# Kernel optimization log

Hardware: AMD Instinct MI355X
Metric: run time of the kernel (lower is better)

## Reference

```python
import jax, jax.numpy as jnp
import numpy as np

# dims
B, C, H, W = 2, 256, 128, 256
P, G = 9, 8            # num_pts, num_groups
GC = C // G            # group_channels


def setup_inputs() -> dict:
    key = jax.random.key(0)
    ks = jax.random.split(key, 8)
    s = 0.02
    return {
        "feats1": jax.random.normal(ks[0], (B, C, H, W), jnp.float32),
        "feats2": jax.random.normal(ks[1], (B, C, H, W), jnp.float32),
        "anchor_points": jax.random.uniform(ks[2], (B, H * W, 2), jnp.float32),
        "norm1_g": jnp.ones((C,), jnp.float32), "norm1_b": jnp.zeros((C,), jnp.float32),
        "norm2_g": jnp.ones((C,), jnp.float32), "norm2_b": jnp.zeros((C,), jnp.float32),
        "Wv": jax.random.normal(ks[3], (C, C), jnp.float32) * s, "bv": jnp.zeros((C,), jnp.float32),
        "Ww": jax.random.normal(ks[4], (C, G * P), jnp.float32) * s, "bw": jnp.zeros((G * P,), jnp.float32),
        "Wk": jax.random.normal(ks[5], (C, P), jnp.float32) * s, "bk": jnp.zeros((P,), jnp.float32),
        "Wo": jax.random.normal(ks[6], (C, C), jnp.float32) * s, "bo": jnp.zeros((C,), jnp.float32),
    }


def _ln(x, g, b):
    # LayerNorm over the last (channel) axis, eps as torch default
    m = jnp.mean(x, axis=-1, keepdims=True)
    v = jnp.mean(jnp.square(x - m), axis=-1, keepdims=True)
    return (x - m) * jax.lax.rsqrt(v + 1e-5) * g + b


def _bilinear_sample(value, pts):
    # value: (b, H, W, C); pts: (b, N, 2) normalized [0,1] (x, y)
    # grid_sample semantics: align_corners=False, zero padding
    b, h, w, c = value.shape
    x = pts[..., 0] * w - 0.5
    y = pts[..., 1] * h - 0.5
    x0 = jnp.floor(x)
    y0 = jnp.floor(y)
    wx = (x - x0)[..., None]
    wy = (y - y0)[..., None]
    x0i = x0.astype(jnp.int32)
    y0i = y0.astype(jnp.int32)
    vflat = value.reshape(b, h * w, c)

    def gather(yi, xi):
        valid = (yi >= 0) & (yi < h) & (xi >= 0) & (xi < w)
        idx = jnp.clip(yi, 0, h - 1) * w + jnp.clip(xi, 0, w - 1)
        g = jnp.take_along_axis(vflat, idx[..., None], axis=1)
        return g * valid[..., None].astype(value.dtype)

    v00 = gather(y0i, x0i)
    v01 = gather(y0i, x0i + 1)
    v10 = gather(y0i + 1, x0i)
    v11 = gather(y0i + 1, x0i + 1)
    return (v00 * (1 - wx) * (1 - wy) + v01 * wx * (1 - wy)
            + v10 * (1 - wx) * wy + v11 * wx * wy)


def reference(feats1, feats2, anchor_points, norm1_g, norm1_b, norm2_g, norm2_b,
              Wv, bv, Ww, bw, Wk, bk, Wo, bo):
    b, c, h, w = feats1.shape
    hw = h * w
    # to_3d(dim=2): (b, c, h, w) -> (b, hw, c); LayerNorm over c
    x1 = _ln(feats1.reshape(b, c, hw).transpose(0, 2, 1), norm1_g, norm1_b)
    x2 = _ln(feats2.reshape(b, c, hw).transpose(0, 2, 1), norm2_g, norm2_b)

    # value_proj (1x1 conv == per-pixel linear)
    value = (x2 @ Wv + bv).reshape(b, h, w, c)

    # weight_proj -> (b, hw, P, G); channel layout p*G + g; softmax over the P points per group
    logits = (x1 @ Ww + bw).reshape(b, hw, P, G)
    wts = jax.nn.softmax(logits, axis=2)

    # 1D key-point generator: per-pixel learned offsets along x around the anchor
    off = x1 @ Wk + bk                                   # (b, hw, P) normalized offsets
    kx = anchor_points[..., 0:1] + off                   # (b, hw, P)
    ky = jnp.broadcast_to(anchor_points[..., 1:2], kx.shape)
    kp = jnp.stack([kx, ky], axis=-1)                    # (b, hw, P, 2)

    # deformable aggregation: bilinear gather + group-weighted sum over points
    samp = _bilinear_sample(value, kp.reshape(b, hw * P, 2)).reshape(b, hw, P, G, GC)
    agg = jnp.einsum('bnpgc,bnpg->bngc', samp, wts).reshape(b, hw, c)

    out = (agg @ Wo + bo).reshape(b, h, w, c).transpose(0, 3, 1, 2)  # (b, c, h, w)
    return out, kp.reshape(b, h, w, P, 2)
```

## Files before the change

### kernel.cpp

```cpp
#include <hip/hip_runtime.h>
#include <hip/hip_bf16.h>


constexpr int B = 2, C = 256, H = 128, W = 256;
constexpr int HW = H * W;
constexpr int P = 9, G = 8;
constexpr int PIX = 32;
constexpr int NPIX = B * HW;
constexpr int NBKT = 2 * 129;

typedef __attribute__((ext_vector_type(8))) __bf16 bf16x8;
typedef __attribute__((ext_vector_type(4))) float f32x4;
typedef __attribute__((ext_vector_type(2))) float f32x2;
typedef __attribute__((ext_vector_type(2))) __fp16 fp16x2;

static __device__ __forceinline__ unsigned short f2bf(float x) {
    __hip_bfloat16 h = __float2bfloat16(x);
    return *reinterpret_cast<unsigned short*>(&h);
}
static __device__ __forceinline__ unsigned int pack2(float a, float b) {
    return (unsigned int)f2bf(a) | ((unsigned int)f2bf(b) << 16);
}
static __device__ __forceinline__ unsigned int pkh(float a, float b) {
    fp16x2 h = __builtin_amdgcn_cvt_pkrtz(a, b);
    return *reinterpret_cast<unsigned int*>(&h);
}
static __device__ __forceinline__ float bf2f(unsigned short u) {
    return __uint_as_float((unsigned int)u << 16);
}
static __device__ __forceinline__ bf16x8 ldb8g(const unsigned short* p) {
    return *reinterpret_cast<const bf16x8*>(p);
}

#define FMA_LO(acc, pk, c) \
    asm("v_fma_mix_f32 %0, %1, %2, %0 op_sel:[0,0,0] op_sel_hi:[1,0,0]" \
        : "+v"(acc) : "v"(pk), "v"(c))
#define FMA_HI(acc, pk, c) \
    asm("v_fma_mix_f32 %0, %1, %2, %0 op_sel:[1,0,0] op_sel_hi:[1,0,0]" \
        : "+v"(acc) : "v"(pk), "v"(c))

__global__ __launch_bounds__(256) void k_prep(
    const float* __restrict__ Ww, const float* __restrict__ Wv,
    const float* __restrict__ Wo,
    unsigned short* __restrict__ WwT, unsigned short* __restrict__ WvT,
    unsigned short* __restrict__ WoT)
{
    int tid = blockIdx.x * 256 + threadIdx.x;
    if (tid < 20480) {
        int n = tid >> 8, k = tid & 255;
        WwT[tid] = f2bf((n < 72) ? Ww[k * 72 + n] : 0.f);
    } else if (tid < 20480 + 65536) {
        int i = tid - 20480;
        int n = i >> 8, k = i & 255;
        WvT[i] = f2bf(Wv[k * 256 + n]);
    } else {
        int i = tid - 86016;
        int n = i >> 8, k = i & 255;
        WoT[i] = f2bf(Wo[k * 256 + n]);
    }
}

static __device__ __forceinline__ int bucket_of(const float* anchor, int pix) {
    float ay = anchor[(size_t)pix * 2 + 1];
    int y0 = (int)floorf(ay * (float)H - 0.5f);
    y0 = min(max(y0, -1), H - 1);
    return (pix >> 15) * 129 + y0 + 1;
}

__global__ __launch_bounds__(1024) void k_hist(
    const float* __restrict__ anchor, int* __restrict__ hist64)
{
    __shared__ int h[NBKT];
    const int t = threadIdx.x, blk = blockIdx.x;
    for (int i = t; i < NBKT; i += 1024) h[i] = 0;
    __syncthreads();
    atomicAdd(&h[bucket_of(anchor, blk * 1024 + t)], 1);
    __syncthreads();
    for (int i = t; i < NBKT; i += 1024) hist64[blk * NBKT + i] = h[i];
}

__global__ __launch_bounds__(256) void k_scan(
    const int* __restrict__ hist64, int* __restrict__ off)
{
    __shared__ int tot[NBKT], base[NBKT];
    const int t = threadIdx.x;
    for (int bkt = t; bkt < NBKT; bkt += 256) {
        int run = 0;
        for (int blk = 0; blk < 64; ++blk) run += hist64[blk * NBKT + bkt];
        tot[bkt] = run;
    }
    __syncthreads();
    if (t == 0) {
        int run = 0;
        for (int i = 0; i < NBKT; ++i) { base[i] = run; run += tot[i]; }
    }
    __syncthreads();
    for (int bkt = t; bkt < NBKT; bkt += 256) {
        int run = base[bkt];
        for (int blk = 0; blk < 64; ++blk) {
            int v = hist64[blk * NBKT + bkt];
            off[blk * NBKT + bkt] = run;
            run += v;
        }
    }
}

__global__ __launch_bounds__(1024) void k_scatter(
    const float* __restrict__ anchor, const int* __restrict__ off,
    int* __restrict__ perm)
{
    __shared__ int cur[NBKT];
    const int t = threadIdx.x, blk = blockIdx.x;
    for (int i = t; i < NBKT; i += 1024) cur[i] = off[blk * NBKT + i];
    __syncthreads();
    int pix = blk * 1024 + t;
    int pos = atomicAdd(&cur[bucket_of(anchor, pix)], 1);
    perm[pos] = pix;
}

__global__ __launch_bounds__(256) void kA(
    const float* __restrict__ feats1, const float* __restrict__ anchor,
    const float* __restrict__ g1, const float* __restrict__ b1,
    const float* __restrict__ Wk, const float* __restrict__ bk,
    const unsigned short* __restrict__ WwT, const float* __restrict__ bw,
    unsigned short* __restrict__ wtsb, float* __restrict__ kp_out)
{
    __shared__ unsigned short Hi[PIX][264];
    __shared__ __align__(16) char smB[20480];
    __shared__ float meanA[PIX], rstdA[PIX], axL[PIX], ayL[PIX];

    float* WkL  = (float*)smB;
    float* red2 = (float*)(smB + 9216);
    float* red  = (float*)(smB + 18432);
    float* Lg   = (float*)smB;

    const int t = threadIdx.x;
    const int p = t & 31;
    const int part = t >> 5;
    const int gpix0 = blockIdx.x * PIX;
    const int b = gpix0 >> 15;
    const int n0 = gpix0 & (HW - 1);
    const float* Fb = feats1 + (size_t)b * C * HW;

    for (int i = t; i < 2304; i += 256) WkL[i] = Wk[i];
    if (t < PIX) {
        axL[t] = anchor[((size_t)gpix0 + t) * 2 + 0];
        ayL[t] = anchor[((size_t)gpix0 + t) * 2 + 1];
    }

    float x[32];
    #pragma unroll
    for (int i = 0; i < 32; ++i)
        x[i] = Fb[(size_t)(part * 32 + i) * HW + n0 + p];

    float s = 0.f, ss = 0.f;
    #pragma unroll
    for (int i = 0; i < 32; ++i) { s += x[i]; ss += x[i] * x[i]; }
    red[part * 32 + p] = s;
    red[256 + part * 32 + p] = ss;
    __syncthreads();
    if (part == 0) {
        float s2 = 0.f, ss2 = 0.f;
        #pragma unroll
        for (int k = 0; k < 8; ++k) { s2 += red[k * 32 + p]; ss2 += red[256 + k * 32 + p]; }
        float mean = s2 * (1.f / C);
        float var  = ss2 * (1.f / C) - mean * mean;
        meanA[p] = mean; rstdA[p] = rsqrtf(var + 1e-5f);
    }
    __syncthreads();

    {
        float mean = meanA[p], rstd = rstdA[p];
        #pragma unroll
        for (int i = 0; i < 32; ++i) {
            int c = part * 32 + i;
            x[i] = (x[i] - mean) * rstd * g1[c] + b1[c];
        }
    }

    {
        float po[9];
        #pragma unroll
        for (int pt = 0; pt < 9; ++pt) po[pt] = 0.f;
        #pragma unroll 4
        for (int i = 0; i < 32; ++i) {
            int c = part * 32 + i;
            float xv = x[i];
            #pragma unroll
            for (int pt = 0; pt < 9; ++pt) po[pt] += xv * WkL[c * 9 + pt];
        }
        #pragma unroll
        for (int pt = 0; pt < 9; ++pt) red2[(part * 32 + p) * 9 + pt] = po[pt];
    }

    {
        unsigned int* row = (unsigned int*)&Hi[p][part * 32];
        #pragma unroll
        for (int i = 0; i < 16; ++i) row[i] = pack2(x[2 * i], x[2 * i + 1]);
    }
    __syncthreads();

    for (int tau = t; tau < 288; tau += 256) {
        int px = tau & 31, pt = tau >> 5;
        float offv = bk[pt];
        #pragma unroll
        for (int k = 0; k < 8; ++k) offv += red2[(k * 32 + px) * 9 + pt];
        size_t o = (((size_t)gpix0 + px) * P + pt) * 2;
        kp_out[o] = axL[px] + offv;
        kp_out[o + 1] = ayL[px];
    }

    const int wave = t >> 6, lane = t & 63;
    const int l15 = lane & 15, quad = lane >> 4;
    const int mt = wave & 1;
    const int ntb = (wave >> 1) * 3;
    const int ntc = (wave >> 1) ? 2 : 3;

    f32x4 acc[3];
    #pragma unroll
    for (int j = 0; j < 3; ++j) acc[j] = (f32x4){0.f, 0.f, 0.f, 0.f};

    const unsigned short* arow = &Hi[mt * 16 + l15][quad * 8];
    for (int kk = 0; kk < 8; ++kk) {
        bf16x8 a = *reinterpret_cast<const bf16x8*>(arow + kk * 32);
        for (int j = 0; j < 3; ++j) {
            if (j < ntc) {
                bf16x8 bfr = ldb8g(WwT + (size_t)((ntb + j) * 16 + l15) * 256 + quad * 8 + kk * 32);
                acc[j] = __builtin_amdgcn_mfma_f32_16x16x32_bf16(a, bfr, acc[j], 0, 0, 0);
            }
        }
    }
    __syncthreads();

    #pragma unroll
    for (int j = 0; j < 3; ++j) {
        if (j < ntc) {
            int n = (ntb + j) * 16 + l15;
            if (n < 72) {
                float bwn = bw[n];
                #pragma unroll
                for (int r = 0; r < 4; ++r)
                    Lg[(mt * 16 + quad * 4 + r) * 81 + n] = acc[j][r] + bwn;
            }
        }
    }
    __syncthreads();

    {
        int px = t >> 3, g = t & 7;
        float m = -1e30f;
        #pragma unroll
        for (int pt = 0; pt < P; ++pt) m = fmaxf(m, Lg[px * 81 + pt * 8 + g]);
        float e[P], sum = 0.f;
        #pragma unroll
        for (int pt = 0; pt < P; ++pt) { e[pt] = __expf(Lg[px * 81 + pt * 8 + g] - m); sum += e[pt]; }
        float inv = 1.f / sum;
        unsigned short* wb = wtsb + ((size_t)gpix0 + px) * 72 + g * 9;
        #pragma unroll
        for (int pt = 0; pt < P; ++pt) wb[pt] = f2bf(e[pt] * inv);
    }
}

__global__ __launch_bounds__(256) void kB(
    const float* __restrict__ feats2,
    const float* __restrict__ g2, const float* __restrict__ b2,
    const unsigned short* __restrict__ WvT, const float* __restrict__ bv,
    unsigned short* __restrict__ val)
{
    __shared__ unsigned short Hi[PIX][264];
    __shared__ float red[2][8][PIX];
    __shared__ float meanA[PIX], rstdA[PIX];

    const int t = threadIdx.x;
    const int p = t & 31;
    const int part = t >> 5;
    const int gpix0 = blockIdx.x * PIX;
    const int b = gpix0 >> 15;
    const int n0 = gpix0 & (HW - 1);
    const float* Fb = feats2 + (size_t)b * C * HW;

    float x[32];
    #pragma unroll
    for (int i = 0; i < 32; ++i)
        x[i] = Fb[(size_t)(part * 32 + i) * HW + n0 + p];

    float s = 0.f, ss = 0.f;
    #pragma unroll
    for (int i = 0; i < 32; ++i) { s += x[i]; ss += x[i] * x[i]; }
    red[0][part][p] = s; red[1][part][p] = ss;
    __syncthreads();
    if (part == 0) {
        float s2 = 0.f, ss2 = 0.f;
        #pragma unroll
        for (int k = 0; k < 8; ++k) { s2 += red[0][k][p]; ss2 += red[1][k][p]; }
        float mean = s2 * (1.f / C);
        float var  = ss2 * (1.f / C) - mean * mean;
        meanA[p] = mean; rstdA[p] = rsqrtf(var + 1e-5f);
    }
    __syncthreads();
    {
        float mean = meanA[p], rstd = rstdA[p];
        unsigned int* row = (unsigned int*)&Hi[p][part * 32];
        #pragma unroll
        for (int i = 0; i < 16; ++i) {
            float v0 = (x[2 * i] - mean) * rstd * g2[part * 32 + 2 * i] + b2[part * 32 + 2 * i];
            float v1 = (x[2 * i + 1] - mean) * rstd * g2[part * 32 + 2 * i + 1] + b2[part * 32 + 2 * i + 1];
            row[i] = pack2(v0, v1);
        }
    }
    __syncthreads();

    const int wave = t >> 6, lane = t & 63;
    const int l15 = lane & 15, quad = lane >> 4;
    const int m0 = wave * 64;

    f32x4 acc[4][2];
    #pragma unroll
    for (int ms = 0; ms < 4; ++ms)
        #pragma unroll
        for (int nt = 0; nt < 2; ++nt)
            acc[ms][nt] = (f32x4){0.f, 0.f, 0.f, 0.f};

    for (int kk = 0; kk < 8; ++kk) {
        bf16x8 a[4], bfr[2];
        #pragma unroll
        for (int ms = 0; ms < 4; ++ms)
            a[ms] = ldb8g(WvT + (size_t)(m0 + ms * 16 + l15) * 256 + quad * 8 + kk * 32);
        #pragma unroll
        for (int nt = 0; nt < 2; ++nt)
            bfr[nt] = *reinterpret_cast<const bf16x8*>(&Hi[nt * 16 + l15][quad * 8 + kk * 32]);
        #pragma unroll
        for (int ms = 0; ms < 4; ++ms)
            #pragma unroll
            for (int nt = 0; nt < 2; ++nt)
                acc[ms][nt] = __builtin_amdgcn_mfma_f32_16x16x32_bf16(a[ms], bfr[nt], acc[ms][nt], 0, 0, 0);
    }

    #pragma unroll
    for (int ms = 0; ms < 4; ++ms) {
        int ch0 = m0 + ms * 16 + quad * 4;
        float b0 = bv[ch0], b1v = bv[ch0 + 1], b2v = bv[ch0 + 2], b3 = bv[ch0 + 3];
        #pragma unroll
        for (int nt = 0; nt < 2; ++nt) {
            int pix = gpix0 + nt * 16 + l15;
            uint2 o;
            o.x = pkh(acc[ms][nt][0] + b0, acc[ms][nt][1] + b1v);
            o.y = pkh(acc[ms][nt][2] + b2v, acc[ms][nt][3] + b3);
            *reinterpret_cast<uint2*>(val + (size_t)pix * 256 + ch0) = o;
        }
    }
}

__global__ __launch_bounds__(256, 4) void k_gather(
    const unsigned short* __restrict__ wtsb,
    const float* __restrict__ kp,
    const unsigned short* __restrict__ val,
    const int* __restrict__ perm,
    unsigned short* __restrict__ aggb)
{
    __shared__ int   CF[PIX][66];
    __shared__ float WL[PIX * 8 * 11];
    __shared__ float EY[PIX][2];
    __shared__ int pixL[PIX];

    const int t = threadIdx.x;
    const int phys = blockIdx.x;
    const int lb = (phys & 7) * 256 + (phys >> 3);
    const int gpix0 = lb * PIX;

    if (t < PIX) {
        int pix = perm[gpix0 + t];
        pixL[t] = pix;
        float ay = kp[(size_t)pix * 18 + 1];
        float yf = ay * (float)H - 0.5f;
        float y0f = floorf(yf);
        float wy = yf - y0f;
        int y0 = (int)y0f;
        EY[t][0] = (((unsigned)y0 < (unsigned)H) ? 1.f : 0.f) * (1.f - wy);
        EY[t][1] = (((unsigned)(y0 + 1) < (unsigned)H) ? 1.f : 0.f) * wy;
        int yb0 = min(max(y0, 0), H - 1) * W;
        int yb1 = min(max(y0 + 1, 0), H - 1) * W;
        int base = (pix >> 15) * HW;
        CF[t][54] = (base + yb0) << 9;
        CF[t][55] = (base + yb1) << 9;
    }
    __syncthreads();

    for (int tau = t; tau < 288; tau += 256) {
        int px = tau & 31, pt = tau >> 5;
        int pix = pixL[px];
        float kx = kp[(size_t)pix * 18 + 2 * pt];
        float e0 = EY[px][0], e1 = EY[px][1];
        float xf = kx * (float)W - 0.5f;
        float x0f = floorf(xf);
        float wx = xf - x0f;
        int x0 = (int)x0f;
        float g0 = (1.f - wx) * (((unsigned)x0 < (unsigned)W) ? 1.f : 0.f);
        float g1v = wx * (((unsigned)(x0 + 1) < (unsigned)W) ? 1.f : 0.f);
        CF[px][pt * 6 + 0] = __float_as_int(g0 * e0);
        CF[px][pt * 6 + 1] = __float_as_int(g1v * e0);
        CF[px][pt * 6 + 2] = __float_as_int(g0 * e1);
        CF[px][pt * 6 + 3] = __float_as_int(g1v * e1);
        CF[px][pt * 6 + 4] = min(max(x0, 0), W - 1) << 9;
        CF[px][pt * 6 + 5] = min(max(x0 + 1, 0), W - 1) << 9;
    }
    {
        int px = t >> 3, j = t & 7;
        int pix = pixL[px];
        const unsigned short* wrow = wtsb + (size_t)pix * 72 + j * 9;
        float* wl = &WL[(px * 8 + j) * 11];
        #pragma unroll
        for (int k = 0; k < 9; ++k) wl[k] = bf2f(wrow[k]);
    }
    __syncthreads();

    const int wave = t >> 6, lane = t & 63;
    const int gl = lane >> 3;
    const char* vb = (const char*)val;
    const unsigned lane8 = (unsigned)lane * 8u;

    for (int px = wave; px < PIX; px += 4) {
        int cw = CF[px][lane];
        unsigned rb0 = (unsigned)__builtin_amdgcn_readlane(cw, 54);
        unsigned rb1 = (unsigned)__builtin_amdgcn_readlane(cw, 55);
        const char* pr0 = vb + rb0;
        const char* pr1 = vb + rb1;
        const float* wl = &WL[(px * 8 + gl) * 11];

        uint2 q[9][4];
        #pragma unroll
        for (int pt = 0; pt < P; ++pt) {
            unsigned xb0 = (unsigned)__builtin_amdgcn_readlane(cw, pt * 6 + 4);
            unsigned xb1 = (unsigned)__builtin_amdgcn_readlane(cw, pt * 6 + 5);
            q[pt][0] = *(const uint2*)(pr0 + xb0 + lane8);
            q[pt][1] = *(const uint2*)(pr0 + xb1 + lane8);
            q[pt][2] = *(const uint2*)(pr1 + xb0 + lane8);
            q[pt][3] = *(const uint2*)(pr1 + xb1 + lane8);
        }

        float a0 = 0.f, a1 = 0.f, a2 = 0.f, a3 = 0.f;
        #pragma unroll
        for (int pt = 0; pt < P; ++pt) {
            float u00 = __int_as_float(__builtin_amdgcn_readlane(cw, pt * 6 + 0));
            float u01 = __int_as_float(__builtin_amdgcn_readlane(cw, pt * 6 + 1));
            float u10 = __int_as_float(__builtin_amdgcn_readlane(cw, pt * 6 + 2));
            float u11 = __int_as_float(__builtin_amdgcn_readlane(cw, pt * 6 + 3));
            float w = wl[pt];
            float c00 = w * u00, c01 = w * u01, c10 = w * u10, c11 = w * u11;

            FMA_LO(a0, q[pt][0].x, c00); FMA_HI(a1, q[pt][0].x, c00);
            FMA_LO(a2, q[pt][0].y, c00); FMA_HI(a3, q[pt][0].y, c00);
            FMA_LO(a0, q[pt][1].x, c01); FMA_HI(a1, q[pt][1].x, c01);
            FMA_LO(a2, q[pt][1].y, c01); FMA_HI(a3, q[pt][1].y, c01);
            FMA_LO(a0, q[pt][2].x, c10); FMA_HI(a1, q[pt][2].x, c10);
            FMA_LO(a2, q[pt][2].y, c10); FMA_HI(a3, q[pt][2].y, c10);
            FMA_LO(a0, q[pt][3].x, c11); FMA_HI(a1, q[pt][3].x, c11);
            FMA_LO(a2, q[pt][3].y, c11); FMA_HI(a3, q[pt][3].y, c11);
        }

        int pix = pixL[px];
        uint2 o;
        o.x = pack2(a0, a1);
        o.y = pack2(a2, a3);
        *reinterpret_cast<uint2*>(aggb + ((size_t)pix << 8) + 4 * lane) = o;
    }
}

__global__ __launch_bounds__(256) void k_gemmo(
    const unsigned short* __restrict__ aggb,
    const unsigned short* __restrict__ WoT,
    const float* __restrict__ bo,
    float* __restrict__ out)
{
    const int t = threadIdx.x;
    const int wave = t >> 6, lane = t & 63;
    const int n_base = blockIdx.x * 64;
    const int b = n_base >> 15;
    const int hw0 = n_base & (HW - 1);
    const int m0 = wave * 64;
    const int l15 = lane & 15, quad = lane >> 4;

    f32x4 acc[4][4];
    #pragma unroll
    for (int ms = 0; ms < 4; ++ms)
        #pragma unroll
        for (int ns = 0; ns < 4; ++ns)
            acc[ms][ns] = (f32x4){0.f, 0.f, 0.f, 0.f};

    size_t aoff[4], boff[4];
    #pragma unroll
    for (int ms = 0; ms < 4; ++ms)
        aoff[ms] = (size_t)(m0 + ms * 16 + l15) * 256 + quad * 8;
    #pragma unroll
    for (int ns = 0; ns < 4; ++ns)
        boff[ns] = (size_t)(n_base + ns * 16 + l15) * 256 + quad * 8;

    for (int kk = 0; kk < 8; ++kk) {
        bf16x8 a[4], bfr[4];
        #pragma unroll
        for (int ms = 0; ms < 4; ++ms) a[ms] = ldb8g(WoT + aoff[ms] + kk * 32);
        #pragma unroll
        for (int ns = 0; ns < 4; ++ns) bfr[ns] = ldb8g(aggb + boff[ns] + kk * 32);
        #pragma unroll
        for (int ms = 0; ms < 4; ++ms)
            #pragma unroll
            for (int ns = 0; ns < 4; ++ns)
                acc[ms][ns] = __builtin_amdgcn_mfma_f32_16x16x32_bf16(a[ms], bfr[ns], acc[ms][ns], 0, 0, 0);
    }

    float bor[4][4];
    #pragma unroll
    for (int ms = 0; ms < 4; ++ms)
        #pragma unroll
        for (int r = 0; r < 4; ++r)
            bor[ms][r] = bo[m0 + ms * 16 + quad * 4 + r];

    #pragma unroll
    for (int ms = 0; ms < 4; ++ms) {
        #pragma unroll
        for (int ns = 0; ns < 4; ++ns) {
            #pragma unroll
            for (int r = 0; r < 4; ++r) {
                int ch = m0 + ms * 16 + quad * 4 + r;
                out[((size_t)b * 256 + ch) * HW + hw0 + ns * 16 + l15] = acc[ms][ns][r] + bor[ms][r];
            }
        }
    }
}

extern "C" void kernel_launch(void* const* d_in, const int* in_sizes, int n_in,
                              void* d_out, int out_size, void* d_ws, size_t ws_size,
                              hipStream_t stream)
{
    const float* feats1 = (const float*)d_in[0];
    const float* feats2 = (const float*)d_in[1];
    const float* anchor = (const float*)d_in[2];
    const float* n1g    = (const float*)d_in[3];
    const float* n1b    = (const float*)d_in[4];
    const float* n2g    = (const float*)d_in[5];
    const float* n2b    = (const float*)d_in[6];
    const float* Wv     = (const float*)d_in[7];
    const float* bv     = (const float*)d_in[8];
    const float* Ww     = (const float*)d_in[9];
    const float* bw     = (const float*)d_in[10];
    const float* Wk     = (const float*)d_in[11];
    const float* bk     = (const float*)d_in[12];
    const float* Wo     = (const float*)d_in[13];
    const float* bo     = (const float*)d_in[14];

    float* out = (float*)d_out;
    float* kp  = out + (size_t)B * C * HW;

    char* ws = (char*)d_ws;
    unsigned short* val  = (unsigned short*)(ws);
    unsigned short* aggb = (unsigned short*)(ws + 33554432);
    unsigned short* wtsb = (unsigned short*)(ws + 67108864);
    unsigned short* WwT  = (unsigned short*)(ws + 76546048);
    unsigned short* WvT  = (unsigned short*)(ws + 76587008);
    unsigned short* WoT  = (unsigned short*)(ws + 76718080);
    int* perm   = (int*)(ws + 76849152);
    int* hist64 = (int*)(ws + 77111296);
    int* off    = (int*)(ws + 77375488);

    k_prep   <<<592,  256,  0, stream>>>(Ww, Wv, Wo, WwT, WvT, WoT);
    k_hist   <<<64,   1024, 0, stream>>>(anchor, hist64);
    k_scan   <<<1,    256,  0, stream>>>(hist64, off);
    k_scatter<<<64,   1024, 0, stream>>>(anchor, off, perm);
    kA       <<<2048, 256,  0, stream>>>(feats1, anchor, n1g, n1b, Wk, bk, WwT, bw, wtsb, kp);
    kB       <<<2048, 256,  0, stream>>>(feats2, n2g, n2b, WvT, bv, val);
    k_gather <<<2048, 256,  0, stream>>>(wtsb, kp, val, perm, aggb);
    k_gemmo  <<<1024, 256,  0, stream>>>(aggb, WoT, bo, out);
}
```

Baseline: 404.5 us.

## Software-pipeline gather loads across pixels in deformable aggregation kernel

New measurement: 404.2 us. No clear change (-0.1%).

```diff
diff --git a/kernel.cpp b/kernel.cpp
--- a/kernel.cpp
+++ b/kernel.cpp
@@ -348,6 +348,47 @@
             o.y = pkh(acc[ms][nt][2] + b2v, acc[ms][nt][3] + b3);
             *reinterpret_cast<uint2*>(val + (size_t)pix * 256 + ch0) = o;
         }
+    }
+}
+
+template <int PTBASE, int NPT>
+static __device__ __forceinline__ void issue_loads(
+    uint2* q, int cw, const char* pr0, const char* pr1, unsigned lane8)
+{
+    #pragma unroll
+    for (int j = 0; j < NPT; ++j) {
+        unsigned xb0 = (unsigned)__builtin_amdgcn_readlane(cw, (PTBASE + j) * 6 + 4);
+        unsigned xb1 = (unsigned)__builtin_amdgcn_readlane(cw, (PTBASE + j) * 6 + 5);
+        q[4 * j + 0] = *(const uint2*)(pr0 + xb0 + lane8);
+        q[4 * j + 1] = *(const uint2*)(pr0 + xb1 + lane8);
+        q[4 * j + 2] = *(const uint2*)(pr1 + xb0 + lane8);
+        q[4 * j + 3] = *(const uint2*)(pr1 + xb1 + lane8);
+    }
+}
+
+template <int PTBASE, int NPT>
+static __device__ __forceinline__ void fma_block(
+    const uint2* q, int cw, const float* wl,
+    float& a0, float& a1, float& a2, float& a3)
+{
+    #pragma unroll
+    for (int j = 0; j < NPT; ++j) {
+        const int pt = PTBASE + j;
+        float u00 = __int_as_float(__builtin_amdgcn_readlane(cw, pt * 6 + 0));
+        float u01 = __int_as_float(__builtin_amdgcn_readlane(cw, pt * 6 + 1));
+        float u10 = __int_as_float(__builtin_amdgcn_readlane(cw, pt * 6 + 2));
+        float u11 = __int_as_float(__builtin_amdgcn_readlane(cw, pt * 6 + 3));
+        float w = wl[pt];
+        float c00 = w * u00, c01 = w * u01, c10 = w * u10, c11 = w * u11;
+
+        FMA_LO(a0, q[4 * j + 0].x, c00); FMA_HI(a1, q[4 * j + 0].x, c00);
+        FMA_LO(a2, q[4 * j + 0].y, c00); FMA_HI(a3, q[4 * j + 0].y, c00);
+        FMA_LO(a0, q[4 * j + 1].x, c01); FMA_HI(a1, q[4 * j + 1].x, c01);
+        FMA_LO(a2, q[4 * j + 1].y, c01); FMA_HI(a3, q[4 * j + 1].y, c01);
+        FMA_LO(a0, q[4 * j + 2].x, c10); FMA_HI(a1, q[4 * j + 2].x, c10);
+        FMA_LO(a2, q[4 * j + 2].y, c10); FMA_HI(a3, q[4 * j + 2].y, c10);
+        FMA_LO(a0, q[4 * j + 3].x, c11); FMA_HI(a1, q[4 * j + 3].x, c11);
+        FMA_LO(a2, q[4 * j + 3].y, c11); FMA_HI(a3, q[4 * j + 3].y, c11);
     }
 }
 
@@ -419,50 +460,51 @@
     const char* vb = (const char*)val;
     const unsigned lane8 = (unsigned)lane * 8u;
 
-    for (int px = wave; px < PIX; px += 4) {
-        int cw = CF[px][lane];
-        unsigned rb0 = (unsigned)__builtin_amdgcn_readlane(cw, 54);
-        unsigned rb1 = (unsigned)__builtin_amdgcn_readlane(cw, 55);
+    uint2 qa[16], qb[20];
+
+    int px = wave;
+    int cwA = CF[px][lane];
+    {
+        unsigned rb0 = (unsigned)__builtin_amdgcn_readlane(cwA, 54);
+        unsigned rb1 = (unsigned)__builtin_amdgcn_readlane(cwA, 55);
         const char* pr0 = vb + rb0;
         const char* pr1 = vb + rb1;
+        issue_loads<0, 4>(qa, cwA, pr0, pr1, lane8);
+    }
+    unsigned rbA0 = (unsigned)__builtin_amdgcn_readlane(cwA, 54);
+    unsigned rbA1 = (unsigned)__builtin_amdgcn_readlane(cwA, 55);
+
+    for (int i = 0; i < 8; ++i) {
         const float* wl = &WL[(px * 8 + gl) * 11];
-
-        uint2 q[9][4];
-        #pragma unroll
-        for (int pt = 0; pt < P; ++pt) {
-            unsigned xb0 = (unsigned)__builtin_amdgcn_readlane(cw, pt * 6 + 4);
-            unsigned xb1 = (unsigned)__builtin_amdgcn_readlane(cw, pt * 6 + 5);
-            q[pt][0] = *(const uint2*)(pr0 + xb0 + lane8);
-            q[pt][1] = *(const uint2*)(pr0 + xb1 + lane8);
-            q[pt][2] = *(const uint2*)(pr1 + xb0 + lane8);
-            q[pt][3] = *(const uint2*)(pr1 + xb1 + lane8);
-        }
+        const char* pr0A = vb + rbA0;
+        const char* pr1A = vb + rbA1;
+
+        issue_loads<4, 5>(qb, cwA, pr0A, pr1A, lane8);
+        __builtin_amdgcn_sched_barrier(0);
 
         float a0 = 0.f, a1 = 0.f, a2 = 0.f, a3 = 0.f;
-        #pragma unroll
-        for (int pt = 0; pt < P; ++pt) {
-            float u00 = __int_as_float(__builtin_amdgcn_readlane(cw, pt * 6 + 0));
-            float u01 = __int_as_float(__builtin_amdgcn_readlane(cw, pt * 6 + 1));
-            float u10 = __int_as_float(__builtin_amdgcn_readlane(cw, pt * 6 + 2));
-            float u11 = __int_as_float(__builtin_amdgcn_readlane(cw, pt * 6 + 3));
-            float w = wl[pt];
-            float c00 = w * u00, c01 = w * u01, c10 = w * u10, c11 = w * u11;
-
-            FMA_LO(a0, q[pt][0].x, c00); FMA_HI(a1, q[pt][0].x, c00);
-            FMA_LO(a2, q[pt][0].y, c00); FMA_HI(a3, q[pt][0].y, c00);
-            FMA_LO(a0, q[pt][1].x, c01); FMA_HI(a1, q[pt][1].x, c01);
-            FMA_LO(a2, q[pt][1].y, c01); FMA_HI(a3, q[pt][1].y, c01);
-            FMA_LO(a0, q[pt][2].x, c10); FMA_HI(a1, q[pt][2].x, c10);
-            FMA_LO(a2, q[pt][2].y, c10); FMA_HI(a3, q[pt][2].y, c10);
-            FMA_LO(a0, q[pt][3].x, c11); FMA_HI(a1, q[pt][3].x, c11);
-            FMA_LO(a2, q[pt][3].y, c11); FMA_HI(a3, q[pt][3].y, c11);
-        }
+        fma_block<0, 4>(qa, cwA, wl, a0, a1, a2, a3);
+
+        int pxn = (i < 7) ? px + 4 : px;
+        int cwN = CF[pxn][lane];
+        unsigned rbN0 = (unsigned)__builtin_amdgcn_readlane(cwN, 54);
+        unsigned rbN1 = (unsigned)__builtin_amdgcn_readlane(cwN, 55);
+        {
+            const char* pr0N = vb + rbN0;
+            const char* pr1N = vb + rbN1;
+            issue_loads<0, 4>(qa, cwN, pr0N, pr1N, lane8);
+        }
+        __builtin_amdgcn_sched_barrier(0);
+
+        fma_block<4, 5>(qb, cwA, wl, a0, a1, a2, a3);
 
         int pix = pixL[px];
         uint2 o;
         o.x = pack2(a0, a1);
         o.y = pack2(a2, a3);
         *reinterpret_cast<uint2*>(aggb + ((size_t)pix << 8) + 4 * lane) = o;
+
+        cwA = cwN; rbA0 = rbN0; rbA1 = rbN1; px = pxn;
     }
 }
 
```
